# Optimization experiments

Hardware: AMD Instinct MI355X
Metric: run time of the kernel (lower is better)

The kernel has to match this reference:

```python
import jax, jax.numpy as jnp
import numpy as np

ITERATIONS = 3
OUT_CAPS, OUT_DIM = 10, 16


def squash(x):
    # square_norm / (1 + square_norm) * x / (sqrt(square_norm) + 1e-6), norm over last axis
    sn = jnp.sum(x * x, axis=-1, keepdims=True)
    return sn / (1.0 + sn) * x / (jnp.sqrt(sn) + 1e-6)


def setup_inputs() -> dict:
    key = jax.random.key(0)
    kx, kw = jax.random.split(key)
    x = jax.random.normal(kx, (256, 32, 6, 6, 8), dtype=jnp.float32)
    W = 0.01 * jax.random.normal(kw, (1, 32, 6, 6, 10, 8, 16), dtype=jnp.float32)
    return {"x": x, "W": W}


def reference(x, W):
    w = W[0]  # [i,j,k,o,d,e]
    # u_hat: prediction vectors, [B, i, j, k, O, E]
    u_hat = jnp.einsum('bijkd,ijkode->bijkoe', x, w)
    u_det = jax.lax.stop_gradient(u_hat)
    b = jnp.zeros(u_hat.shape[:-1], dtype=u_hat.dtype)  # [B,i,j,k,O]
    for _ in range(ITERATIONS - 1):
        c = jax.nn.softmax(b, axis=-1)
        s = jnp.einsum('bijko,bijkoe->boe', c, u_det)   # reduce over all input-capsule axes
        v = squash(s)                                    # [B,O,E]
        b = b + jnp.einsum('bijkoe,boe->bijko', u_det, v)
    c = jax.nn.softmax(b, axis=-1)
    s = jnp.einsum('bijko,bijkoe->boe', c, u_hat)
    v = squash(s)
    return v.reshape(-1, OUT_CAPS, OUT_DIM)
```

## Files before the change

kernel.cpp:

```cpp
#include <hip/hip_runtime.h>
#include <math.h>

#define BATCH 256
#define IC    1152
#define DD    8
#define OO    10
#define EE    16
#define BTILE 64
#define NBT   4
#define NT    640
#define CHUNK 9
#define NCHUNK 128

__global__ __launch_bounds__(NT) void caps_pass_kernel(
    const float* __restrict__ x,
    const float* __restrict__ W,
    const float* __restrict__ V,
    float* __restrict__ s_part,
    int first)
{
    __shared__ float x_lds[CHUNK][DD][BTILE];
    __shared__ float v_lds[OO][EE][BTILE];
    __shared__ float elg_lds[2][NT];

    const int tid = threadIdx.x;
    const int o   = tid >> 6;
    const int bl  = tid & 63;
    const int o_u = __builtin_amdgcn_readfirstlane(o);
    const int b   = blockIdx.y * BTILE + bl;
    const int ijk0 = blockIdx.x * CHUNK;

    {
        const float* xgrp = x + (size_t)(blockIdx.y * BTILE) * (IC * DD);
        #pragma unroll 1
        for (int i = tid; i < CHUNK * BTILE * 2; i += NT) {
            const int lq = i & 1;
            const int lb = (i >> 1) & 63;
            const int ls = i >> 7;
            const float4 t = *reinterpret_cast<const float4*>(
                xgrp + (size_t)lb * (IC * DD) + (size_t)(ijk0 + ls) * DD + lq * 4);
            x_lds[ls][lq * 4 + 0][lb] = t.x;
            x_lds[ls][lq * 4 + 1][lb] = t.y;
            x_lds[ls][lq * 4 + 2][lb] = t.z;
            x_lds[ls][lq * 4 + 3][lb] = t.w;
        }
    }

    if (!first) {
        const float4* vp = reinterpret_cast<const float4*>(V + ((size_t)b * OO + o) * EE);
        #pragma unroll
        for (int q = 0; q < 4; ++q) {
            const float4 t = vp[q];
            v_lds[o][q * 4 + 0][bl] = t.x;
            v_lds[o][q * 4 + 1][bl] = t.y;
            v_lds[o][q * 4 + 2][bl] = t.z;
            v_lds[o][q * 4 + 3][bl] = t.w;
        }
    }
    __syncthreads();

    float sacc[EE];
    #pragma unroll
    for (int e = 0; e < EE; ++e) sacc[e] = 0.f;

    int p = 0;
    #pragma unroll 1
    for (int s = 0; s < CHUNK; ++s) {
        const float* wp = W + (size_t)(ijk0 + s) * (OO * DD * EE) + o_u * (DD * EE);

        float u[EE];
        #pragma unroll
        for (int e = 0; e < EE; ++e) u[e] = 0.f;
        #pragma unroll
        for (int d = 0; d < DD; ++d) {
            const float xv = x_lds[s][d][bl];
            #pragma unroll
            for (int e = 0; e < EE; ++e)
                u[e] = fmaf(xv, wp[d * EE + e], u[e]);
        }

        float c;
        if (!first) {
            float lg = 0.f;
            #pragma unroll
            for (int e = 0; e < EE; ++e)
                lg = fmaf(u[e], v_lds[o][e][bl], lg);
            const float elg = __expf(lg);
            elg_lds[p][tid] = elg;
            __syncthreads();
            float den = 0.f;
            #pragma unroll
            for (int oo = 0; oo < OO; ++oo)
                den += elg_lds[p][oo * 64 + bl];
            c = __fdividef(elg, den);
            p ^= 1;
        } else {
            c = 1.0f;
        }

        #pragma unroll
        for (int e = 0; e < EE; ++e)
            sacc[e] = fmaf(c, u[e], sacc[e]);
    }

    const float mul = first ? 0.1f : 1.0f;
    float* sp = s_part + (((size_t)blockIdx.x * BATCH + b) * OO + o) * EE;
    #pragma unroll
    for (int q = 0; q < 4; ++q) {
        float4 t;
        t.x = mul * sacc[q * 4 + 0]; t.y = mul * sacc[q * 4 + 1];
        t.z = mul * sacc[q * 4 + 2]; t.w = mul * sacc[q * 4 + 3];
        reinterpret_cast<float4*>(sp)[q] = t;
    }
}

__global__ __launch_bounds__(256) void caps_squash_kernel(
    const float* __restrict__ s_part,
    float* __restrict__ V,
    float* __restrict__ out,
    int accum, int last)
{
    __shared__ float red[3][64];
    const int lane = threadIdx.x & 63;
    const int w    = threadIdx.x >> 6;
    const int g    = blockIdx.x * 64 + lane;

    const float* sp = s_part + g;
    float s = 0.f;
    #pragma unroll 8
    for (int ch = w * (NCHUNK / 4); ch < (w + 1) * (NCHUNK / 4); ++ch)
        s += sp[(size_t)ch * (BATCH * OO * EE)];

    if (w > 0) red[w - 1][lane] = s;
    __syncthreads();
    if (w == 0) {
        s += red[0][lane] + red[1][lane] + red[2][lane];

        float sq = s * s;
        #pragma unroll
        for (int m = 1; m < 16; m <<= 1) sq += __shfl_xor(sq, m, 16);

        float scale = sq / (1.f + sq) / (sqrtf(sq) + 1e-6f);
        float v = scale * s;

        if (last)       out[g] = v;
        else if (accum) V[g]  += v;
        else            V[g]   = v;
    }
}

extern "C" void kernel_launch(void* const* d_in, const int* in_sizes, int n_in,
                              void* d_out, int out_size, void* d_ws, size_t ws_size,
                              hipStream_t stream) {
    const float* x = (const float*)d_in[0];
    const float* W = (const float*)d_in[1];
    float* out = (float*)d_out;

    float* s_part = (float*)d_ws;
    float* V      = s_part + (size_t)NCHUNK * BATCH * OO * EE;

    dim3 grid(NCHUNK, NBT), blk(NT);
    const int sq_blocks = (BATCH * OO * EE) / 64;

    caps_pass_kernel<<<grid, blk, 0, stream>>>(x, W, V, s_part, 1);
    caps_squash_kernel<<<sq_blocks, 256, 0, stream>>>(s_part, V, out, 0, 0);
    caps_pass_kernel<<<grid, blk, 0, stream>>>(x, W, V, s_part, 0);
    caps_squash_kernel<<<sq_blocks, 256, 0, stream>>>(s_part, V, out, 1, 0);
    caps_pass_kernel<<<grid, blk, 0, stream>>>(x, W, V, s_part, 0);
    caps_squash_kernel<<<sq_blocks, 256, 0, stream>>>(s_part, V, out, 0, 1);
}
```

Before: 166.3 us.

## Stage W chunk in LDS, keep V in registers, rebalance chunk count

Each block now cooperatively copies its chunk of W into shared memory with float4 loads and reads it from LDS as float4 broadcasts, instead of issuing scalar global loads per output capsule. The V vector is kept in per-thread registers instead of a shared transposed array. CHUNK drops to 8 and NCHUNK rises to 144, so W fits in LDS and the grid gets more blocks. The trade-off is larger partial-sum buffers for the squash reduction, higher register pressure, and the extra LDS occupancy cost of 40KB of W.

```diff
diff --git a/kernel.cpp b/kernel.cpp
--- a/kernel.cpp
+++ b/kernel.cpp
@@ -9,8 +9,9 @@
 #define BTILE 64
 #define NBT   4
 #define NT    640
-#define CHUNK 9
-#define NCHUNK 128
+#define CHUNK 8
+#define NCHUNK 144
+#define WPC   (OO * DD * EE)
 
 __global__ __launch_bounds__(NT) void caps_pass_kernel(
     const float* __restrict__ x,
@@ -19,16 +20,23 @@
     float* __restrict__ s_part,
     int first)
 {
+    __shared__ float w_lds[CHUNK][WPC];
     __shared__ float x_lds[CHUNK][DD][BTILE];
-    __shared__ float v_lds[OO][EE][BTILE];
     __shared__ float elg_lds[2][NT];
 
     const int tid = threadIdx.x;
     const int o   = tid >> 6;
     const int bl  = tid & 63;
-    const int o_u = __builtin_amdgcn_readfirstlane(o);
     const int b   = blockIdx.y * BTILE + bl;
     const int ijk0 = blockIdx.x * CHUNK;
+
+    {
+        const float4* wg = reinterpret_cast<const float4*>(W + (size_t)ijk0 * WPC);
+        float4* wl = reinterpret_cast<float4*>(&w_lds[0][0]);
+        #pragma unroll
+        for (int i = 0; i < (CHUNK * WPC / 4) / NT; ++i)
+            wl[tid + i * NT] = wg[tid + i * NT];
+    }
 
     {
         const float* xgrp = x + (size_t)(blockIdx.y * BTILE) * (IC * DD);
@@ -46,15 +54,14 @@
         }
     }
 
+    float vreg[EE];
     if (!first) {
         const float4* vp = reinterpret_cast<const float4*>(V + ((size_t)b * OO + o) * EE);
         #pragma unroll
         for (int q = 0; q < 4; ++q) {
-            const float4 t = vp[q];
-            v_lds[o][q * 4 + 0][bl] = t.x;
-            v_lds[o][q * 4 + 1][bl] = t.y;
-            v_lds[o][q * 4 + 2][bl] = t.z;
-            v_lds[o][q * 4 + 3][bl] = t.w;
+            float4 t = vp[q];
+            vreg[q * 4 + 0] = t.x; vreg[q * 4 + 1] = t.y;
+            vreg[q * 4 + 2] = t.z; vreg[q * 4 + 3] = t.w;
         }
     }
     __syncthreads();
@@ -66,7 +73,7 @@
     int p = 0;
     #pragma unroll 1
     for (int s = 0; s < CHUNK; ++s) {
-        const float* wp = W + (size_t)(ijk0 + s) * (OO * DD * EE) + o_u * (DD * EE);
+        const float4* wq = reinterpret_cast<const float4*>(&w_lds[s][o * (DD * EE)]);
 
         float u[EE];
         #pragma unroll
@@ -75,16 +82,20 @@
         for (int d = 0; d < DD; ++d) {
             const float xv = x_lds[s][d][bl];
             #pragma unroll
-            for (int e = 0; e < EE; ++e)
-                u[e] = fmaf(xv, wp[d * EE + e], u[e]);
+            for (int q = 0; q < 4; ++q) {
+                const float4 w4 = wq[d * 4 + q];
+                u[q * 4 + 0] = fmaf(xv, w4.x, u[q * 4 + 0]);
+                u[q * 4 + 1] = fmaf(xv, w4.y, u[q * 4 + 1]);
+                u[q * 4 + 2] = fmaf(xv, w4.z, u[q * 4 + 2]);
+                u[q * 4 + 3] = fmaf(xv, w4.w, u[q * 4 + 3]);
+            }
         }
 
         float c;
         if (!first) {
             float lg = 0.f;
             #pragma unroll
-            for (int e = 0; e < EE; ++e)
-                lg = fmaf(u[e], v_lds[o][e][bl], lg);
+            for (int e = 0; e < EE; ++e) lg = fmaf(u[e], vreg[e], lg);
             const float elg = __expf(lg);
             elg_lds[p][tid] = elg;
             __syncthreads();
@@ -127,7 +138,7 @@
 
     const float* sp = s_part + g;
     float s = 0.f;
-    #pragma unroll 8
+    #pragma unroll 4
     for (int ch = w * (NCHUNK / 4); ch < (w + 1) * (NCHUNK / 4); ++ch)
         s += sp[(size_t)ch * (BATCH * OO * EE)];
 
```

Result: slower. 184.8 us (+11.1%).
